# Kernel tuning notes

Hardware: AMD Instinct MI355X
Metric: run time of the kernel (lower is better)

The kernel has to match this reference:

```python
import jax, jax.numpy as jnp
import numpy as np

B, S = 16, 8192
Q_DIM, K_DIM, ATTN_DIM = 512, 512, 512


def setup_inputs() -> dict:
    key = jax.random.key(0)
    k1, k2, k3, k4, k5, k6 = jax.random.split(key, 6)
    query = jax.random.normal(k1, (B, Q_DIM), dtype=jnp.float32)
    keys = jax.random.normal(k2, (B, S, K_DIM), dtype=jnp.float32)
    mask = jax.random.randint(k3, (B, S), 0, 2, dtype=jnp.int32)
    # learned params (torch Linear stores weight as [out, in]; we keep [in, out])
    Wq = jax.random.normal(k4, (Q_DIM, ATTN_DIM), dtype=jnp.float32) / np.sqrt(Q_DIM)
    Wk = jax.random.normal(k5, (K_DIM, ATTN_DIM), dtype=jnp.float32) / np.sqrt(K_DIM)
    v = jax.random.normal(k6, (ATTN_DIM,), dtype=jnp.float32) / np.sqrt(ATTN_DIM)
    return {"query": query, "keys": keys, "mask": mask, "Wq": Wq, "Wk": Wk, "v": v}


def reference(query, keys, mask, Wq, Wk, v):
    # q: [B, 1, A], k: [B, S, A]
    q = (query @ Wq)[:, None, :]
    k = jnp.einsum('bsk,ka->bsa', keys, Wk)
    # scores e: [B, S]  (v-projection reduces attn dim)
    e = jnp.einsum('bsa,a->bs', jnp.tanh(q + k), v)
    neg_min = jnp.finfo(e.dtype).min
    e = jnp.where(mask == 0, neg_min, e)
    a = jax.nn.softmax(e, axis=-1)  # [B, S]
    c = jnp.einsum('bs,bsk->bk', a, keys)  # context [B, K_DIM]
    return (c, a)
```

## Files before the change

### kernel.cpp

```cpp
#include <hip/hip_runtime.h>

#define BB 16
#define SS 8192
#define DD 512

typedef float  f32x4  __attribute__((ext_vector_type(4)));
typedef __bf16 bf16x8 __attribute__((ext_vector_type(8)));
typedef __bf16 bf16x4 __attribute__((ext_vector_type(4)));

__device__ __forceinline__ void cvt_store_bf4(unsigned short* dst, f32x4 v) {
    bf16x4 o;
    o.x = (__bf16)v.x; o.y = (__bf16)v.y; o.z = (__bf16)v.z; o.w = (__bf16)v.w;
    *(bf16x4*)dst = o;
}

__device__ __forceinline__ float tanh_fast(float x) {
    float e2 = __expf(2.0f * x);
    return 1.0f - 2.0f / (e2 + 1.0f);
}

__global__ __launch_bounds__(256) void prep_kernel(
    const float* __restrict__ query, const float* __restrict__ Wq,
    const float* __restrict__ Wk, float* __restrict__ qproj,
    unsigned short* __restrict__ WkT_f)
{
    __shared__ __bf16 lt[64][65];
    const int bid = blockIdx.x, t = threadIdx.x;
    if (bid < 64) {
        const int k0 = (bid >> 3) * 64, n0 = (bid & 7) * 64;
#pragma unroll
        for (int rep = 0; rep < 4; ++rep) {
            const int k = rep * 16 + (t >> 4), n = (t & 15) * 4;
            f32x4 vv = *(const f32x4*)&Wk[(size_t)(k0 + k) * DD + n0 + n];
            lt[k][n] = (__bf16)vv.x; lt[k][n + 1] = (__bf16)vv.y;
            lt[k][n + 2] = (__bf16)vv.z; lt[k][n + 3] = (__bf16)vv.w;
        }
        __syncthreads();
        const int g_loc = t >> 6, lane = t & 63;
        const int ml = lane & 15, quad = lane >> 4;
        const int g = (bid & 7) * 4 + g_loc;
#pragma unroll
        for (int j_loc = 0; j_loc < 2; ++j_loc) {
            const int j = (bid >> 3) * 2 + j_loc;
            bf16x8 o;
#pragma unroll
            for (int d = 0; d < 8; ++d)
                o[d] = lt[j_loc * 32 + quad * 8 + d][g_loc * 16 + ml];
            *(bf16x8*)&WkT_f[((size_t)((g * 16 + j) * 64 + lane)) * 8] = o;
        }
    } else {
        const int idx = (bid - 64) * 256 + t;
        const int b = idx >> 9;
        const int n = idx & 511;
        const float* q  = query + b * DD;
        const float* wp = Wq + n;
        float acc = 0.0f;
#pragma unroll 8
        for (int k = 0; k < DD; ++k)
            acc = fmaf(q[k], wp[(size_t)k * DD], acc);
        qproj[b * DD + n] = acc;
    }
}

__global__ __launch_bounds__(512, 4) void fused_kernel(
    const float* __restrict__ keys, const unsigned short* __restrict__ WkT_f,
    const float* __restrict__ qproj, const float* __restrict__ vvec,
    const int* __restrict__ mask, float* __restrict__ e_ws,
    float* __restrict__ cpart, float2* __restrict__ ml_ws)
{
    __shared__ unsigned short ksA[16 * 2048];
    __shared__ float sm_part[8][64];
    __shared__ float w_sh[64];
    __shared__ f32x4 red[3][128];

    const int tid  = threadIdx.x;
    const int w    = tid >> 6;
    const int lane = tid & 63;
    const int ml   = lane & 15;
    const int quad = lane >> 4;
    const int bid  = blockIdx.x;
    const int b    = bid >> 7;
    const int chunk = bid & 127;
    const int s0   = chunk << 6;

    int mk = 0;
    if (tid < 64) mk = mask[(size_t)b * SS + s0 + tid];

    const int m  = tid >> 3;
    const int q8 = tid & 7;
    const float* krow = keys + ((size_t)(b * SS + s0 + m)) * DD + q8 * 4;
    const int it = m >> 4;
    const int sq = q8 >> 1;
    const int j0 = (q8 & 1) * 4;
    const int base = it * 512 + ((m & 15) + 16 * sq) * 8 + j0;
    {
        f32x4 kst[8];
#pragma unroll
        for (int h = 0; h < 2; ++h) {
#pragma unroll
            for (int j = 0; j < 8; ++j)
                kst[j] = __builtin_nontemporal_load(
                             (const f32x4*)(krow + (h * 8 + j) * 32));
#pragma unroll
            for (int j = 0; j < 8; ++j)
                cvt_store_bf4(&ksA[(h * 8 + j) * 2048 + base], kst[j]);
        }
    }
    __syncthreads();

    const unsigned short* wfb = WkT_f + (size_t)w * 32768 + lane * 8;

    f32x4 acc[4][4];
#pragma unroll
    for (int i = 0; i < 4; ++i)
#pragma unroll
        for (int jn = 0; jn < 4; ++jn) acc[i][jn] = (f32x4){0.f, 0.f, 0.f, 0.f};

#pragma unroll 4
    for (int j = 0; j < 16; ++j) {
        bf16x8 af[4];
#pragma unroll
        for (int i = 0; i < 4; ++i)
            af[i] = *(const bf16x8*)&ksA[j * 2048 + (i * 64 + lane) * 8];
#pragma unroll
        for (int jn = 0; jn < 4; ++jn) {
            bf16x8 bfr = *(const bf16x8*)(wfb + ((jn * 16 + j) << 9));
#pragma unroll
            for (int i = 0; i < 4; ++i)
                acc[i][jn] = __builtin_amdgcn_mfma_f32_16x16x32_bf16(af[i], bfr, acc[i][jn], 0, 0, 0);
        }
    }

    float qv[4], vv[4];
#pragma unroll
    for (int jn = 0; jn < 4; ++jn) {
        const int n = w * 64 + jn * 16 + ml;
        qv[jn] = qproj[b * DD + n];
        vv[jn] = vvec[n];
    }
#pragma unroll
    for (int i = 0; i < 4; ++i) {
#pragma unroll
        for (int r = 0; r < 4; ++r) {
            float s = 0.0f;
#pragma unroll
            for (int jn = 0; jn < 4; ++jn) {
                float xx = acc[i][jn][r] + qv[jn];
                s += tanh_fast(xx) * vv[jn];
            }
            s += __shfl_xor(s, 1, 64);
            s += __shfl_xor(s, 2, 64);
            s += __shfl_xor(s, 4, 64);
            s += __shfl_xor(s, 8, 64);
            if (ml == 0) sm_part[w][i * 16 + quad * 4 + r] = s;
        }
    }
    __syncthreads();

    if (tid < 64) {
        float e = sm_part[0][tid] + sm_part[1][tid] + sm_part[2][tid] + sm_part[3][tid]
                + sm_part[4][tid] + sm_part[5][tid] + sm_part[6][tid] + sm_part[7][tid];
        if (mk == 0) e = -3.402823466e38f;
        e_ws[(size_t)b * SS + s0 + tid] = e;
        float mx = e;
#pragma unroll
        for (int off = 32; off >= 1; off >>= 1) mx = fmaxf(mx, __shfl_xor(mx, off, 64));
        float wv = (mk == 0) ? 0.0f : __expf(e - mx);
        float l  = wv;
#pragma unroll
        for (int off = 32; off >= 1; off >>= 1) l += __shfl_xor(l, off, 64);
        w_sh[tid] = wv;
        if (tid == 0) ml_ws[b * 128 + chunk] = make_float2(mx, l);
    }
    __syncthreads();

    const int l   = tid & 127;
    const int sh  = tid >> 7;
    const int n4  = l << 2;
    const int jq  = l >> 3;
    const int qd  = (l >> 1) & 3;
    const int d0  = (l & 1) * 4;
    const int cbase = jq * 2048 + sh * 512 + qd * 128 + d0;
    const int rot   = (l & 15) + (l >> 3);
    f32x4 cacc = (f32x4){0.f, 0.f, 0.f, 0.f};
#pragma unroll
    for (int p = 0; p < 16; ++p) {
        const int sI = (p + rot) & 15;
        bf16x4 kv = *(const bf16x4*)&ksA[cbase + sI * 8];
        const float wgt = w_sh[sh * 16 + sI];
        cacc.x += wgt * (float)kv.x;
        cacc.y += wgt * (float)kv.y;
        cacc.z += wgt * (float)kv.z;
        cacc.w += wgt * (float)kv.w;
    }
    if (sh) red[sh - 1][l] = cacc;
    __syncthreads();
    if (sh == 0) {
        cacc += red[0][l] + red[1][l] + red[2][l];
        *(f32x4*)(cpart + ((size_t)(b * 128 + chunk)) * 512 + n4) = cacc;
    }
}

__global__ __launch_bounds__(256) void finalize_kernel(
    const float* __restrict__ e_ws, const float* __restrict__ cpart,
    const float2* __restrict__ ml_ws, float* __restrict__ out)
{
    __shared__ float rm[4], rs[4];
    __shared__ float sc_sh[128];
    __shared__ float cred[4][512];
    const int bid = blockIdx.x, t = threadIdx.x;
    const int b = (bid < 16) ? bid : ((bid - 16) >> 3);

    float mi = -3.402823466e38f, li = 0.0f;
    if (t < 128) { float2 p = ml_ws[b * 128 + t]; mi = p.x; li = p.y; }
    float mr = mi;
#pragma unroll
    for (int off = 32; off >= 1; off >>= 1) mr = fmaxf(mr, __shfl_xor(mr, off, 64));
    if ((t & 63) == 0) rm[t >> 6] = mr;
    __syncthreads();
    const float M = fmaxf(fmaxf(rm[0], rm[1]), fmaxf(rm[2], rm[3]));
    float si = (t < 128) ? li * __expf(mi - M) : 0.0f;
#pragma unroll
    for (int off = 32; off >= 1; off >>= 1) si += __shfl_xor(si, off, 64);
    if ((t & 63) == 0) rs[t >> 6] = si;
    __syncthreads();
    const float L = rs[0] + rs[1] + rs[2] + rs[3];
    const float invL = 1.0f / L;

    if (bid < 16) {
        if (t < 128) sc_sh[t] = __expf(ml_ws[b * 128 + t].x - M);
        __syncthreads();
        const int w2 = t >> 6, l = t & 63;
        float pa[8] = {0.f, 0.f, 0.f, 0.f, 0.f, 0.f, 0.f, 0.f};
#pragma unroll 4
        for (int i = w2 * 32; i < w2 * 32 + 32; ++i) {
            const float sc = sc_sh[i];
            const float* cp = cpart + ((size_t)(b * 128 + i)) * 512 + l * 8;
#pragma unroll
            for (int c = 0; c < 8; ++c) pa[c] = fmaf(cp[c], sc, pa[c]);
        }
#pragma unroll
        for (int c = 0; c < 8; ++c) cred[w2][l * 8 + c] = pa[c];
        __syncthreads();
#pragma unroll
        for (int rep = 0; rep < 2; ++rep) {
            const int n = t + rep * 256;
            out[b * DD + n] = (cred[0][n] + cred[1][n] + cred[2][n] + cred[3][n]) * invL;
        }
    } else {
        const int chunk8 = (bid - 16) & 7;
        const float* ep = e_ws + (size_t)b * SS + chunk8 * 1024;
        float* ap = out + BB * DD + (size_t)b * SS + chunk8 * 1024;
#pragma unroll
        for (int r = 0; r < 4; ++r) {
            float e = ep[t + 256 * r];
            ap[t + 256 * r] = __expf(e - M) * invL;
        }
    }
}

extern "C" void kernel_launch(void* const* d_in, const int* in_sizes, int n_in,
                              void* d_out, int out_size, void* d_ws, size_t ws_size,
                              hipStream_t stream)
{
    const float* query = (const float*)d_in[0];
    const float* keys  = (const float*)d_in[1];
    const int*   mask  = (const int*)  d_in[2];
    const float* Wq    = (const float*)d_in[3];
    const float* Wk    = (const float*)d_in[4];
    const float* v     = (const float*)d_in[5];
    float* out = (float*)d_out;

    float*          qproj = (float*)d_ws;
    unsigned short* WkT_f = (unsigned short*)((char*)d_ws + 32768);
    float*          e_ws  = (float*)((char*)d_ws + 32768 + 524288);
    float*          cpart = (float*)((char*)d_ws + 32768 + 2 * 524288);
    float2*         ml_ws = (float2*)((char*)d_ws + 32768 + 2 * 524288 + 4194304);

    prep_kernel    <<<96, 256, 0, stream>>>(query, Wq, Wk, qproj, WkT_f);
    fused_kernel   <<<BB * (SS / 64), 512, 0, stream>>>(keys, WkT_f, qproj, v, mask,
                                                        e_ws, cpart, ml_ws);
    finalize_kernel<<<16 + 128, 256, 0, stream>>>(e_ws, cpart, ml_ws, out);
}
```

Baseline: 458.5 us.

## Make fused kernel persistent over four chunks with register prefetch of next keys

Each block now handles four consecutive 64-row chunks of one batch instead of one, cutting the grid from 2048 to 512 blocks. The next chunk's keys are loaded into registers before the softmax and context phases of the current chunk and written to shared memory afterwards, overlapping global loads with compute. In exchange it holds 16 extra f32x4 registers per thread, which may reduce occupancy under the 512x4 launch bound, and it gives up the parallelism of the larger grid.

```diff
diff --git a/kernel.cpp b/kernel.cpp
--- a/kernel.cpp
+++ b/kernel.cpp
@@ -79,57 +79,24 @@
     const int ml   = lane & 15;
     const int quad = lane >> 4;
     const int bid  = blockIdx.x;
-    const int b    = bid >> 7;
-    const int chunk = bid & 127;
-    const int s0   = chunk << 6;
-
-    int mk = 0;
-    if (tid < 64) mk = mask[(size_t)b * SS + s0 + tid];
+    const int b    = bid >> 5;
+    const int c0   = (bid & 31) << 2;
 
     const int m  = tid >> 3;
     const int q8 = tid & 7;
-    const float* krow = keys + ((size_t)(b * SS + s0 + m)) * DD + q8 * 4;
     const int it = m >> 4;
     const int sq = q8 >> 1;
     const int j0 = (q8 & 1) * 4;
     const int base = it * 512 + ((m & 15) + 16 * sq) * 8 + j0;
-    {
-        f32x4 kst[8];
-#pragma unroll
-        for (int h = 0; h < 2; ++h) {
-#pragma unroll
-            for (int j = 0; j < 8; ++j)
-                kst[j] = __builtin_nontemporal_load(
-                             (const f32x4*)(krow + (h * 8 + j) * 32));
-#pragma unroll
-            for (int j = 0; j < 8; ++j)
-                cvt_store_bf4(&ksA[(h * 8 + j) * 2048 + base], kst[j]);
-        }
-    }
-    __syncthreads();
+    const float* krow0 = keys + ((size_t)(b * SS + c0 * 64 + m)) * DD + q8 * 4;
 
     const unsigned short* wfb = WkT_f + (size_t)w * 32768 + lane * 8;
 
-    f32x4 acc[4][4];
-#pragma unroll
-    for (int i = 0; i < 4; ++i)
-#pragma unroll
-        for (int jn = 0; jn < 4; ++jn) acc[i][jn] = (f32x4){0.f, 0.f, 0.f, 0.f};
-
-#pragma unroll 4
-    for (int j = 0; j < 16; ++j) {
-        bf16x8 af[4];
-#pragma unroll
-        for (int i = 0; i < 4; ++i)
-            af[i] = *(const bf16x8*)&ksA[j * 2048 + (i * 64 + lane) * 8];
-#pragma unroll
-        for (int jn = 0; jn < 4; ++jn) {
-            bf16x8 bfr = *(const bf16x8*)(wfb + ((jn * 16 + j) << 9));
-#pragma unroll
-            for (int i = 0; i < 4; ++i)
-                acc[i][jn] = __builtin_amdgcn_mfma_f32_16x16x32_bf16(af[i], bfr, acc[i][jn], 0, 0, 0);
-        }
-    }
+    const int l   = tid & 127;
+    const int sh  = tid >> 7;
+    const int n4  = l << 2;
+    const int cbase = (l >> 3) * 2048 + sh * 512 + ((l >> 1) & 3) * 128 + (l & 1) * 4;
+    const int rot   = (l & 15) + (l >> 3);
 
     float qv[4], vv[4];
 #pragma unroll
@@ -138,66 +105,123 @@
         qv[jn] = qproj[b * DD + n];
         vv[jn] = vvec[n];
     }
-#pragma unroll
-    for (int i = 0; i < 4; ++i) {
-#pragma unroll
-        for (int r = 0; r < 4; ++r) {
-            float s = 0.0f;
+
+    {
+        f32x4 kst[8];
+#pragma unroll
+        for (int h = 0; h < 2; ++h) {
+#pragma unroll
+            for (int j = 0; j < 8; ++j)
+                kst[j] = __builtin_nontemporal_load(
+                             (const f32x4*)(krow0 + (h * 8 + j) * 32));
+#pragma unroll
+            for (int j = 0; j < 8; ++j)
+                cvt_store_bf4(&ksA[(h * 8 + j) * 2048 + base], kst[j]);
+        }
+    }
+    __syncthreads();
+
+#pragma unroll 1
+    for (int t = 0; t < 4; ++t) {
+        const int c  = c0 + t;
+        const int s0 = c << 6;
+
+        int mk = 0;
+        if (tid < 64) mk = mask[(size_t)b * SS + s0 + tid];
+
+        f32x4 acc[4][4];
+#pragma unroll
+        for (int i = 0; i < 4; ++i)
+#pragma unroll
+            for (int jn = 0; jn < 4; ++jn) acc[i][jn] = (f32x4){0.f, 0.f, 0.f, 0.f};
+
+#pragma unroll 4
+        for (int j = 0; j < 16; ++j) {
+            bf16x8 af[4];
+#pragma unroll
+            for (int i = 0; i < 4; ++i)
+                af[i] = *(const bf16x8*)&ksA[j * 2048 + (i * 64 + lane) * 8];
 #pragma unroll
             for (int jn = 0; jn < 4; ++jn) {
-                float xx = acc[i][jn][r] + qv[jn];
-                s += tanh_fast(xx) * vv[jn];
+                bf16x8 bfr = *(const bf16x8*)(wfb + ((jn * 16 + j) << 9));
+#pragma unroll
+                for (int i = 0; i < 4; ++i)
+                    acc[i][jn] = __builtin_amdgcn_mfma_f32_16x16x32_bf16(af[i], bfr, acc[i][jn], 0, 0, 0);
             }
-            s += __shfl_xor(s, 1, 64);
-            s += __shfl_xor(s, 2, 64);
-            s += __shfl_xor(s, 4, 64);
-            s += __shfl_xor(s, 8, 64);
-            if (ml == 0) sm_part[w][i * 16 + quad * 4 + r] = s;
-        }
-    }
-    __syncthreads();
-
-    if (tid < 64) {
-        float e = sm_part[0][tid] + sm_part[1][tid] + sm_part[2][tid] + sm_part[3][tid]
-                + sm_part[4][tid] + sm_part[5][tid] + sm_part[6][tid] + sm_part[7][tid];
-        if (mk == 0) e = -3.402823466e38f;
-        e_ws[(size_t)b * SS + s0 + tid] = e;
-        float mx = e;
-#pragma unroll
-        for (int off = 32; off >= 1; off >>= 1) mx = fmaxf(mx, __shfl_xor(mx, off, 64));
-        float wv = (mk == 0) ? 0.0f : __expf(e - mx);
-        float l  = wv;
-#pragma unroll
-        for (int off = 32; off >= 1; off >>= 1) l += __shfl_xor(l, off, 64);
-        w_sh[tid] = wv;
-        if (tid == 0) ml_ws[b * 128 + chunk] = make_float2(mx, l);
-    }
-    __syncthreads();
-
-    const int l   = tid & 127;
-    const int sh  = tid >> 7;
-    const int n4  = l << 2;
-    const int jq  = l >> 3;
-    const int qd  = (l >> 1) & 3;
-    const int d0  = (l & 1) * 4;
-    const int cbase = jq * 2048 + sh * 512 + qd * 128 + d0;
-    const int rot   = (l & 15) + (l >> 3);
-    f32x4 cacc = (f32x4){0.f, 0.f, 0.f, 0.f};
-#pragma unroll
-    for (int p = 0; p < 16; ++p) {
-        const int sI = (p + rot) & 15;
-        bf16x4 kv = *(const bf16x4*)&ksA[cbase + sI * 8];
-        const float wgt = w_sh[sh * 16 + sI];
-        cacc.x += wgt * (float)kv.x;
-        cacc.y += wgt * (float)kv.y;
-        cacc.z += wgt * (float)kv.z;
-        cacc.w += wgt * (float)kv.w;
-    }
-    if (sh) red[sh - 1][l] = cacc;
-    __syncthreads();
-    if (sh == 0) {
-        cacc += red[0][l] + red[1][l] + red[2][l];
-        *(f32x4*)(cpart + ((size_t)(b * 128 + chunk)) * 512 + n4) = cacc;
+        }
+
+#pragma unroll
+        for (int i = 0; i < 4; ++i) {
+#pragma unroll
+            for (int r = 0; r < 4; ++r) {
+                float s = 0.0f;
+#pragma unroll
+                for (int jn = 0; jn < 4; ++jn) {
+                    float xx = acc[i][jn][r] + qv[jn];
+                    s += tanh_fast(xx) * vv[jn];
+                }
+                s += __shfl_xor(s, 1, 64);
+                s += __shfl_xor(s, 2, 64);
+                s += __shfl_xor(s, 4, 64);
+                s += __shfl_xor(s, 8, 64);
+                if (ml == 0) sm_part[w][i * 16 + quad * 4 + r] = s;
+            }
+        }
+
+        __builtin_amdgcn_sched_barrier(0);
+        f32x4 kst[16];
+        {
+            const float* knext = krow0 + (size_t)(t + 1) * 32768;
+            if (t < 3) {
+#pragma unroll
+                for (int j = 0; j < 16; ++j)
+                    kst[j] = __builtin_nontemporal_load(
+                                 (const f32x4*)(knext + j * 32));
+            }
+        }
+        __syncthreads();
+
+        if (tid < 64) {
+            float e = sm_part[0][tid] + sm_part[1][tid] + sm_part[2][tid] + sm_part[3][tid]
+                    + sm_part[4][tid] + sm_part[5][tid] + sm_part[6][tid] + sm_part[7][tid];
+            if (mk == 0) e = -3.402823466e38f;
+            e_ws[(size_t)b * SS + s0 + tid] = e;
+            float mx = e;
+#pragma unroll
+            for (int off = 32; off >= 1; off >>= 1) mx = fmaxf(mx, __shfl_xor(mx, off, 64));
+            float wv = (mk == 0) ? 0.0f : __expf(e - mx);
+            float lsum = wv;
+#pragma unroll
+            for (int off = 32; off >= 1; off >>= 1) lsum += __shfl_xor(lsum, off, 64);
+            w_sh[tid] = wv;
+            if (tid == 0) ml_ws[b * 128 + c] = make_float2(mx, lsum);
+        }
+        __syncthreads();
+
+        f32x4 cacc = (f32x4){0.f, 0.f, 0.f, 0.f};
+#pragma unroll
+        for (int p = 0; p < 16; ++p) {
+            const int sI = (p + rot) & 15;
+            bf16x4 kv = *(const bf16x4*)&ksA[cbase + sI * 8];
+            const float wgt = w_sh[sh * 16 + sI];
+            cacc.x += wgt * (float)kv.x;
+            cacc.y += wgt * (float)kv.y;
+            cacc.z += wgt * (float)kv.z;
+            cacc.w += wgt * (float)kv.w;
+        }
+        if (sh) red[sh - 1][l] = cacc;
+        __syncthreads();
+        if (sh == 0) {
+            cacc += red[0][l] + red[1][l] + red[2][l];
+            *(f32x4*)(cpart + ((size_t)(b * 128 + c)) * 512 + n4) = cacc;
+        }
+
+        if (t < 3) {
+#pragma unroll
+            for (int j = 0; j < 16; ++j)
+                cvt_store_bf4(&ksA[j * 2048 + base], kst[j]);
+        }
+        __syncthreads();
     }
 }
 
@@ -278,7 +302,7 @@
     float2*         ml_ws = (float2*)((char*)d_ws + 32768 + 2 * 524288 + 4194304);
 
     prep_kernel    <<<96, 256, 0, stream>>>(query, Wq, Wk, qproj, WkT_f);
-    fused_kernel   <<<BB * (SS / 64), 512, 0, stream>>>(keys, WkT_f, qproj, v, mask,
-                                                        e_ws, cpart, ml_ws);
+    fused_kernel   <<<512, 512, 0, stream>>>(keys, WkT_f, qproj, v, mask,
+                                             e_ws, cpart, ml_ws);
     finalize_kernel<<<16 + 128, 256, 0, stream>>>(e_ws, cpart, ml_ws, out);
 }
```

New measurement: 562.4 us. 22.7% more time.
